# Optimization experiments

Hardware: AMD Instinct MI355X
Metric: run time of the kernel (lower is better)

## Reference

```python
import jax, jax.numpy as jnp
import numpy as np

INPUT_DIM, HIDDEN_DIM, OUTPUT_DIM = 64, 128, 1
BATCH, SEQ_LEN = 256, 512


def setup_inputs() -> dict:
    key = jax.random.key(0)
    ks = jax.random.split(key, 10)
    stdv = 1.0 / np.sqrt(HIDDEN_DIM)
    u = lambda k, shape: jax.random.uniform(k, shape, jnp.float32, -stdv, stdv)
    return {
        "X": jax.random.normal(ks[0], (BATCH, SEQ_LEN, INPUT_DIM), jnp.float32),
        "W": u(ks[1], (INPUT_DIM, 4 * HIDDEN_DIM)),
        "U": u(ks[2], (HIDDEN_DIM, 4 * HIDDEN_DIM)),
        "bias": u(ks[3], (4 * HIDDEN_DIM,)),
        "Wa": u(ks[4], (INPUT_DIM, INPUT_DIM)),
        "Ua": u(ks[5], (2 * HIDDEN_DIM, INPUT_DIM)),
        "ba": u(ks[6], (INPUT_DIM,)),
        "Va": u(ks[7], (INPUT_DIM, INPUT_DIM)),
        "fc_w": u(ks[8], (HIDDEN_DIM, OUTPUT_DIM)),
        "fc_b": u(ks[9], (OUTPUT_DIM,)),
    }


def reference(X, W, U, bias, Wa, Ua, ba, Va, fc_w, fc_b):
    B, T, _ = X.shape
    HS = U.shape[0]

    def step(carry, x_t):
        h, c = carry
        # variable attention over input features
        a_t = jnp.tanh(x_t @ Wa + jnp.concatenate([h, c], axis=1) @ Ua + ba) @ Va
        alpha_t = jax.nn.softmax(a_t, axis=1)
        xg = alpha_t * x_t
        gates = xg @ W + h @ U + bias
        i_t = jax.nn.sigmoid(gates[:, :HS])
        f_t = jax.nn.sigmoid(gates[:, HS:2 * HS])
        g_t = jnp.tanh(gates[:, 2 * HS:3 * HS])
        o_t = jax.nn.sigmoid(gates[:, 3 * HS:])
        c = f_t * c + i_t * g_t
        h = o_t * jnp.tanh(c)
        return (h, c), (h, alpha_t)

    h0 = jnp.zeros((B, HS), X.dtype)
    c0 = jnp.zeros((B, HS), X.dtype)
    (h_t, c_t), (hs, alphas) = jax.lax.scan(step, (h0, c0), jnp.swapaxes(X, 0, 1))
    hidden_seq = jnp.swapaxes(hs, 0, 1)  # [B, T, HS]
    y_pred = h_t @ fc_w + fc_b
    return y_pred, hidden_seq, (h_t, c_t), alphas[-1]
```

## Files before the change

kernel.cpp:

```cpp
#include <hip/hip_runtime.h>


#define TSEQ 512
#define NB   256
#define DIN  64
#define DHS  128
#define LOG2E 1.44269504f

typedef short bf16x8 __attribute__((ext_vector_type(8)));
typedef float f32x4  __attribute__((ext_vector_type(4)));

#define SWZ(off, row) ((off) ^ (((row) & 7) << 4))

__device__ __forceinline__ void bar_lds() {
  asm volatile("s_waitcnt lgkmcnt(0)\n\ts_barrier" ::: "memory");
}

__device__ __forceinline__ float fexp2(float x) { return __builtin_amdgcn_exp2f(x); }
__device__ __forceinline__ float frcp(float x)  { return __builtin_amdgcn_rcpf(x); }
__device__ __forceinline__ float sigm(float x)   { return frcp(1.0f + fexp2(-LOG2E * x)); }
__device__ __forceinline__ float tanh_f(float x) { return 1.0f - 2.0f * frcp(1.0f + fexp2(2.0f * LOG2E * x)); }

__device__ __forceinline__ unsigned short f2bf(float f) {
  return (unsigned short)((__float_as_uint(f) + 0x8000u) >> 16);
}
__device__ __forceinline__ unsigned int pack2(float a, float b) {
  return ((__float_as_uint(a) + 0x8000u) >> 16) | ((__float_as_uint(b) + 0x8000u) & 0xffff0000u);
}
__device__ __forceinline__ float bf2f(unsigned short u) {
  return __uint_as_float(((unsigned int)u) << 16);
}

__global__ __launch_bounds__(512, 2) void valstm_kernel(
    const float* __restrict__ X,  const float* __restrict__ W,  const float* __restrict__ U,
    const float* __restrict__ bias, const float* __restrict__ Wa, const float* __restrict__ Ua,
    const float* __restrict__ ba, const float* __restrict__ Va,
    const float* __restrict__ fcw, const float* __restrict__ fcb,
    float* __restrict__ out)
{
  const int tid = threadIdx.x;
  const int w   = tid >> 6;
  const int l   = tid & 63;
  const int lo  = l & 15;
  const int hi  = l >> 4;
  const int b0  = blockIdx.x * 16;

  __shared__ __align__(16) unsigned short hc[16 * 256];
  __shared__ __align__(16) unsigned short xbuf2[2][16 * 64];
  __shared__ __align__(16) unsigned short ta[16 * 64];
  __shared__ __align__(16) unsigned short ubuf[16 * 64];
  __shared__ __align__(16) float S4[64];
  __shared__ __align__(16) float hf[16 * 128];

  bf16x8 Uf[4][4];
  bf16x8 Wf[4][2];
  float  biasr[4];
  const int hid = 16 * w + lo;
  #pragma unroll
  for (int g = 0; g < 4; ++g) {
    const int j = g * 128 + hid;
    biasr[g] = bias[j];
    #pragma unroll
    for (int kt = 0; kt < 4; ++kt) {
      bf16x8 v;
      #pragma unroll
      for (int e = 0; e < 8; ++e) { const int k = kt * 32 + hi * 8 + e; v[e] = (short)f2bf(U[k * 512 + j]); }
      Uf[g][kt] = v;
    }
    #pragma unroll
    for (int kt = 0; kt < 2; ++kt) {
      bf16x8 v;
      #pragma unroll
      for (int e = 0; e < 8; ++e) { const int k = kt * 32 + hi * 8 + e; v[e] = (short)f2bf(W[k * 512 + j]); }
      Wf[g][kt] = v;
    }
  }

  bf16x8 Uaf[8], Waf[2], Vaf[2];
  float  bar = 0.0f;
  if (w < 4) {
    const int ja = 16 * w + lo;
    bar = ba[ja];
    #pragma unroll
    for (int kt = 0; kt < 8; ++kt) {
      bf16x8 v;
      #pragma unroll
      for (int e = 0; e < 8; ++e) { const int k = kt * 32 + hi * 8 + e; v[e] = (short)f2bf(Ua[k * 64 + ja]); }
      Uaf[kt] = v;
    }
    #pragma unroll
    for (int kt = 0; kt < 2; ++kt) {
      bf16x8 v;
      #pragma unroll
      for (int e = 0; e < 8; ++e) { const int k = kt * 32 + hi * 8 + e; v[e] = (short)f2bf(Wa[k * 64 + ja]); }
      Waf[kt] = v;
    }
    #pragma unroll
    for (int kt = 0; kt < 2; ++kt) {
      bf16x8 v;
      #pragma unroll
      for (int e = 0; e < 8; ++e) { const int k = kt * 32 + hi * 8 + e; v[e] = (short)f2bf(Va[k * 64 + ja]); }
      Vaf[kt] = v;
    }
  }

  int haf_off[4], caf_off[4], xa_off[2];
  #pragma unroll
  for (int kt = 0; kt < 4; ++kt) {
    haf_off[kt] = SWZ(lo * 512 + (kt * 32 + hi * 8) * 2, lo);
    caf_off[kt] = SWZ(lo * 512 + ((kt + 4) * 32 + hi * 8) * 2, lo);
  }
  #pragma unroll
  for (int kt = 0; kt < 2; ++kt)
    xa_off[kt] = SWZ(lo * 128 + (kt * 32 + hi * 8) * 2, lo);
  int ta_st[4], hc_h[4], hc_c[4];
  #pragma unroll
  for (int ri = 0; ri < 4; ++ri) {
    const int rr = hi * 4 + ri;
    ta_st[ri] = SWZ(rr * 128 + (16 * w + lo) * 2, rr);
    hc_h[ri]  = SWZ(rr * 512 + hid * 2, rr);
    hc_c[ri]  = SWZ(rr * 512 + (128 + hid) * 2, rr);
  }
  const int uq_off = SWZ(lo * 128 + (16 * w + hi * 4) * 2, lo);

  *(f32x4*)((char*)hc + tid * 16) = (f32x4){0.f, 0.f, 0.f, 0.f};

  const int xr = tid >> 5;
  const int xc = (tid & 31) * 2;
  const int xst_off = SWZ(xr * 128 + xc * 2, xr);
  const float* xptr = X + (size_t)(b0 + xr) * TSEQ * DIN + xc;
  {
    const float2 v0 = *(const float2*)(xptr + 0 * DIN);
    *(unsigned int*)((char*)xbuf2[0] + xst_off) = pack2(v0.x, v0.y);
  }
  float2 xf = *(const float2*)(xptr + 1 * DIN);

  float cst[4] = {0.f, 0.f, 0.f, 0.f};

  float* outY  = out;
  float* outHS = out + 256;
  float* outHT = out + 256 + (size_t)NB * TSEQ * DHS;
  float* outCT = outHT + NB * DHS;
  float* outAL = outCT + NB * DHS;

  float* hsP[4];
  #pragma unroll
  for (int ri = 0; ri < 4; ++ri)
    hsP[ri] = outHS + (size_t)(b0 + hi * 4 + ri) * TSEQ * DHS + hid;

  bar_lds();

  #pragma unroll 1
  for (int t = 0; t < TSEQ - 1; ++t) {
    const int xoff = (t & 1) << 11;

    bf16x8 haf[4];
    #pragma unroll
    for (int kt = 0; kt < 4; ++kt)
      haf[kt] = *(const bf16x8*)((const char*)hc + haf_off[kt]);

    f32x4 accU[4];
    unsigned long long xq = 0;

    if (w >= 4) {
      #pragma unroll
      for (int g = 0; g < 4; ++g) {
        accU[g] = (f32x4){biasr[g], biasr[g], biasr[g], biasr[g]};
        #pragma unroll
        for (int kt = 0; kt < 4; ++kt)
          accU[g] = __builtin_amdgcn_mfma_f32_16x16x32_bf16(haf[kt], Uf[g][kt], accU[g], 0, 0, 0);
      }
    }
    if (w < 4) {
      __builtin_amdgcn_s_setprio(1);
      xq = *(const unsigned long long*)((const char*)xbuf2[0] + xoff + uq_off);
      f32x4 aa = (f32x4){bar, bar, bar, bar};
      f32x4 ah = (f32x4){0.f, 0.f, 0.f, 0.f};
      f32x4 ac = (f32x4){0.f, 0.f, 0.f, 0.f};
      #pragma unroll
      for (int kt = 0; kt < 2; ++kt) {
        bf16x8 xa = *(const bf16x8*)((const char*)xbuf2[0] + xoff + xa_off[kt]);
        aa = __builtin_amdgcn_mfma_f32_16x16x32_bf16(xa, Waf[kt], aa, 0, 0, 0);
      }
      #pragma unroll
      for (int kt = 0; kt < 4; ++kt)
        ah = __builtin_amdgcn_mfma_f32_16x16x32_bf16(haf[kt], Uaf[kt], ah, 0, 0, 0);
      #pragma unroll
      for (int kt = 0; kt < 4; ++kt) {
        bf16x8 ca = *(const bf16x8*)((const char*)hc + caf_off[kt]);
        ac = __builtin_amdgcn_mfma_f32_16x16x32_bf16(ca, Uaf[kt + 4], ac, 0, 0, 0);
      }
      const f32x4 pre = aa + ah + ac;
      #pragma unroll
      for (int ri = 0; ri < 4; ++ri)
        *(unsigned short*)((char*)ta + ta_st[ri]) = f2bf(tanh_f(pre[ri]));
    }
    bar_lds();

    if (w < 4) {
      f32x4 av = (f32x4){0.f, 0.f, 0.f, 0.f};
      #pragma unroll
      for (int kt = 0; kt < 2; ++kt) {
        bf16x8 tf = *(const bf16x8*)((const char*)ta + xa_off[kt]);
        av = __builtin_amdgcn_mfma_f32_16x16x32_bf16(Vaf[kt], tf, av, 0, 0, 0);
      }
      f32x4 ev;
      #pragma unroll
      for (int ri = 0; ri < 4; ++ri) ev[ri] = fexp2(av[ri] * LOG2E);
      const unsigned int p0 = pack2(ev[0] * bf2f((unsigned short)xq),
                                    ev[1] * bf2f((unsigned short)(xq >> 16)));
      const unsigned int p1 = pack2(ev[2] * bf2f((unsigned short)(xq >> 32)),
                                    ev[3] * bf2f((unsigned short)(xq >> 48)));
      *(unsigned long long*)((char*)ubuf + uq_off) =
          (unsigned long long)p0 | ((unsigned long long)p1 << 32);
      float ps = ev[0] + ev[1] + ev[2] + ev[3];
      ps += __shfl_xor(ps, 16);
      ps += __shfl_xor(ps, 32);
      if (hi == 0) S4[lo * 4 + w] = ps;
      __builtin_amdgcn_s_setprio(0);
    }
    bar_lds();

    const bf16x8 uf0 = *(const bf16x8*)((const char*)ubuf + xa_off[0]);
    const bf16x8 uf1 = *(const bf16x8*)((const char*)ubuf + xa_off[1]);
    f32x4 s4r[4];
    #pragma unroll
    for (int ri = 0; ri < 4; ++ri)
      s4r[ri] = *(const f32x4*)(S4 + (hi * 4 + ri) * 4);

    if (w < 4) {
      #pragma unroll
      for (int g = 0; g < 4; ++g) {
        accU[g] = (f32x4){biasr[g], biasr[g], biasr[g], biasr[g]};
        #pragma unroll
        for (int kt = 0; kt < 4; ++kt)
          accU[g] = __builtin_amdgcn_mfma_f32_16x16x32_bf16(haf[kt], Uf[g][kt], accU[g], 0, 0, 0);
      }
    }
    f32x4 accW[4];
    #pragma unroll
    for (int g = 0; g < 4; ++g) accW[g] = (f32x4){0.f, 0.f, 0.f, 0.f};
    #pragma unroll
    for (int g = 0; g < 4; ++g)
      accW[g] = __builtin_amdgcn_mfma_f32_16x16x32_bf16(uf0, Wf[g][0], accW[g], 0, 0, 0);
    #pragma unroll
    for (int g = 0; g < 4; ++g)
      accW[g] = __builtin_amdgcn_mfma_f32_16x16x32_bf16(uf1, Wf[g][1], accW[g], 0, 0, 0);

    float rinv_[4];
    #pragma unroll
    for (int ri = 0; ri < 4; ++ri)
      rinv_[ri] = frcp(s4r[ri][0] + s4r[ri][1] + s4r[ri][2] + s4r[ri][3]);

    #pragma unroll
    for (int ri = 0; ri < 4; ++ri) {
      const float iv = sigm(accW[0][ri] * rinv_[ri] + accU[0][ri]);
      const float fv = sigm(accW[1][ri] * rinv_[ri] + accU[1][ri]);
      const float gv = tanh_f(accW[2][ri] * rinv_[ri] + accU[2][ri]);
      const float ov = sigm(accW[3][ri] * rinv_[ri] + accU[3][ri]);
      const float cn = fv * cst[ri] + iv * gv;
      const float hv = ov * tanh_f(cn);
      cst[ri] = cn;
      *(unsigned short*)((char*)hc + hc_h[ri]) = f2bf(hv);
      *(unsigned short*)((char*)hc + hc_c[ri]) = f2bf(cn);
      *hsP[ri] = hv;
      hsP[ri] += DHS;
    }

    {
      *(unsigned int*)((char*)xbuf2[0] + (((t + 1) & 1) << 11) + xst_off) = pack2(xf.x, xf.y);
      const int tn = (t + 2 < TSEQ) ? t + 2 : TSEQ - 1;
      xf = *(const float2*)(xptr + tn * DIN);
    }
    bar_lds();
  }

  {
    const int xoff = ((TSEQ - 1) & 1) << 11;

    bf16x8 haf[4];
    #pragma unroll
    for (int kt = 0; kt < 4; ++kt)
      haf[kt] = *(const bf16x8*)((const char*)hc + haf_off[kt]);

    if (w < 4) {
      f32x4 aa = (f32x4){bar, bar, bar, bar};
      f32x4 ah = (f32x4){0.f, 0.f, 0.f, 0.f};
      f32x4 ac = (f32x4){0.f, 0.f, 0.f, 0.f};
      #pragma unroll
      for (int kt = 0; kt < 2; ++kt) {
        bf16x8 xa = *(const bf16x8*)((const char*)xbuf2[0] + xoff + xa_off[kt]);
        aa = __builtin_amdgcn_mfma_f32_16x16x32_bf16(xa, Waf[kt], aa, 0, 0, 0);
      }
      #pragma unroll
      for (int kt = 0; kt < 4; ++kt)
        ah = __builtin_amdgcn_mfma_f32_16x16x32_bf16(haf[kt], Uaf[kt], ah, 0, 0, 0);
      #pragma unroll
      for (int kt = 0; kt < 4; ++kt) {
        bf16x8 ca = *(const bf16x8*)((const char*)hc + caf_off[kt]);
        ac = __builtin_amdgcn_mfma_f32_16x16x32_bf16(ca, Uaf[kt + 4], ac, 0, 0, 0);
      }
      const f32x4 pre = aa + ah + ac;
      #pragma unroll
      for (int ri = 0; ri < 4; ++ri)
        *(unsigned short*)((char*)ta + ta_st[ri]) = f2bf(tanh_f(pre[ri]));
    }
    bar_lds();

    f32x4 evP = (f32x4){0.f, 0.f, 0.f, 0.f};
    if (w < 4) {
      f32x4 av = (f32x4){0.f, 0.f, 0.f, 0.f};
      #pragma unroll
      for (int kt = 0; kt < 2; ++kt) {
        bf16x8 tf = *(const bf16x8*)((const char*)ta + xa_off[kt]);
        av = __builtin_amdgcn_mfma_f32_16x16x32_bf16(Vaf[kt], tf, av, 0, 0, 0);
      }
      #pragma unroll
      for (int ri = 0; ri < 4; ++ri) evP[ri] = fexp2(av[ri] * LOG2E);
      float ps = evP[0] + evP[1] + evP[2] + evP[3];
      ps += __shfl_xor(ps, 16);
      ps += __shfl_xor(ps, 32);
      const unsigned long long xq = *(const unsigned long long*)((const char*)xbuf2[0] + xoff + uq_off);
      const unsigned int p0 = pack2(evP[0] * bf2f((unsigned short)xq),
                                    evP[1] * bf2f((unsigned short)(xq >> 16)));
      const unsigned int p1 = pack2(evP[2] * bf2f((unsigned short)(xq >> 32)),
                                    evP[3] * bf2f((unsigned short)(xq >> 48)));
      *(unsigned long long*)((char*)ubuf + uq_off) =
          (unsigned long long)p0 | ((unsigned long long)p1 << 32);
      if (hi == 0) S4[lo * 4 + w] = ps;
    }
    f32x4 accU[4];
    #pragma unroll
    for (int g = 0; g < 4; ++g) {
      accU[g] = (f32x4){biasr[g], biasr[g], biasr[g], biasr[g]};
      #pragma unroll
      for (int kt = 0; kt < 4; ++kt)
        accU[g] = __builtin_amdgcn_mfma_f32_16x16x32_bf16(haf[kt], Uf[g][kt], accU[g], 0, 0, 0);
    }
    bar_lds();

    if (w < 4) {
      const f32x4 s4v = *(const f32x4*)(S4 + lo * 4);
      const float rA = frcp(s4v[0] + s4v[1] + s4v[2] + s4v[3]);
      *(f32x4*)(outAL + (b0 + lo) * 64 + 16 * w + hi * 4) =
          (f32x4){evP[0] * rA, evP[1] * rA, evP[2] * rA, evP[3] * rA};
    }

    f32x4 accW[4];
    #pragma unroll
    for (int g = 0; g < 4; ++g) accW[g] = (f32x4){0.f, 0.f, 0.f, 0.f};
    #pragma unroll
    for (int kt = 0; kt < 2; ++kt) {
      const bf16x8 uf = *(const bf16x8*)((const char*)ubuf + xa_off[kt]);
      #pragma unroll
      for (int g = 0; g < 4; ++g)
        accW[g] = __builtin_amdgcn_mfma_f32_16x16x32_bf16(uf, Wf[g][kt], accW[g], 0, 0, 0);
    }
    float rinv_[4];
    #pragma unroll
    for (int ri = 0; ri < 4; ++ri) {
      const f32x4 s4v = *(const f32x4*)(S4 + (hi * 4 + ri) * 4);
      rinv_[ri] = frcp(s4v[0] + s4v[1] + s4v[2] + s4v[3]);
    }
    #pragma unroll
    for (int ri = 0; ri < 4; ++ri) {
      const int rr = hi * 4 + ri;
      const float iv = sigm(accW[0][ri] * rinv_[ri] + accU[0][ri]);
      const float fv = sigm(accW[1][ri] * rinv_[ri] + accU[1][ri]);
      const float gv = tanh_f(accW[2][ri] * rinv_[ri] + accU[2][ri]);
      const float ov = sigm(accW[3][ri] * rinv_[ri] + accU[3][ri]);
      const float cn = fv * cst[ri] + iv * gv;
      const float hv = ov * tanh_f(cn);
      *(unsigned short*)((char*)hc + hc_h[ri]) = f2bf(hv);
      *(unsigned short*)((char*)hc + hc_c[ri]) = f2bf(cn);
      *hsP[ri] = hv;
      outHT[(b0 + rr) * DHS + hid] = hv;
      outCT[(b0 + rr) * DHS + hid] = cn;
      hf[rr * 128 + hid] = hv;
    }
  }
  bar_lds();

  if (w < 4) {
    const float fw0 = fcw[l], fw1 = fcw[64 + l];
    const float fb = fcb[0];
    #pragma unroll
    for (int rr = 0; rr < 4; ++rr) {
      const int r = w * 4 + rr;
      float s = hf[r * 128 + l] * fw0 + hf[r * 128 + 64 + l] * fw1;
      #pragma unroll
      for (int msk = 1; msk < 64; msk <<= 1) s += __shfl_xor(s, msk);
      if (l == 0) outY[b0 + r] = s + fb;
    }
  }
}

extern "C" void kernel_launch(void* const* d_in, const int* in_sizes, int n_in,
                              void* d_out, int out_size, void* d_ws, size_t ws_size,
                              hipStream_t stream) {
  const float* X    = (const float*)d_in[0];
  const float* W    = (const float*)d_in[1];
  const float* U    = (const float*)d_in[2];
  const float* bias = (const float*)d_in[3];
  const float* Wa   = (const float*)d_in[4];
  const float* Ua   = (const float*)d_in[5];
  const float* ba   = (const float*)d_in[6];
  const float* Va   = (const float*)d_in[7];
  const float* fcw  = (const float*)d_in[8];
  const float* fcb  = (const float*)d_in[9];
  valstm_kernel<<<16, 512, 0, stream>>>(X, W, U, bias, Wa, Ua, ba, Va, fcw, fcb, (float*)d_out);
}
```

Baseline: 996.9 us.

## Fold exp scale constants into weights and rebalance per-wave work in LSTM step

Pre-scales the gate, attention and Va weights and biases by log2e factors at load time, which removes per-element multiplies before the exp2 calls in activations. Moves the U-matrix MFMA for all waves into the slot between the attention phase and the barrier, so attention waves no longer compute it after the barrier. Gives the X prefetch (now float4 per thread) to the gate-only waves during the attention phase, taking it off the tail of every step. The pre-scaling happens before bf16 rounding, which slightly changes numerics.

```diff
diff --git a/kernel.cpp b/kernel.cpp
--- a/kernel.cpp
+++ b/kernel.cpp
@@ -9,6 +9,7 @@
 
 typedef short bf16x8 __attribute__((ext_vector_type(8)));
 typedef float f32x4  __attribute__((ext_vector_type(4)));
+typedef unsigned long long u64;
 
 #define SWZ(off, row) ((off) ^ (((row) & 7) << 4))
 
@@ -18,8 +19,9 @@
 
 __device__ __forceinline__ float fexp2(float x) { return __builtin_amdgcn_exp2f(x); }
 __device__ __forceinline__ float frcp(float x)  { return __builtin_amdgcn_rcpf(x); }
-__device__ __forceinline__ float sigm(float x)   { return frcp(1.0f + fexp2(-LOG2E * x)); }
-__device__ __forceinline__ float tanh_f(float x) { return 1.0f - 2.0f * frcp(1.0f + fexp2(2.0f * LOG2E * x)); }
+__device__ __forceinline__ float sig3(float x)  { return frcp(1.0f + fexp2(-x)); }
+__device__ __forceinline__ float tanh4(float x) { return 1.0f - 2.0f * frcp(1.0f + fexp2(x)); }
+__device__ __forceinline__ float tanh5(float y) { return 1.0f - 2.0f * frcp(1.0f + fexp2(2.0f * LOG2E * y)); }
 
 __device__ __forceinline__ unsigned short f2bf(float f) {
   return (unsigned short)((__float_as_uint(f) + 0x8000u) >> 16);
@@ -52,6 +54,7 @@
   __shared__ __align__(16) float S4[64];
   __shared__ __align__(16) float hf[16 * 128];
 
+  const float sgate[4] = {LOG2E, LOG2E, 2.0f * LOG2E, LOG2E};
   bf16x8 Uf[4][4];
   bf16x8 Wf[4][2];
   float  biasr[4];
@@ -59,19 +62,20 @@
   #pragma unroll
   for (int g = 0; g < 4; ++g) {
     const int j = g * 128 + hid;
-    biasr[g] = bias[j];
+    const float s = sgate[g];
+    biasr[g] = bias[j] * s;
     #pragma unroll
     for (int kt = 0; kt < 4; ++kt) {
       bf16x8 v;
       #pragma unroll
-      for (int e = 0; e < 8; ++e) { const int k = kt * 32 + hi * 8 + e; v[e] = (short)f2bf(U[k * 512 + j]); }
+      for (int e = 0; e < 8; ++e) { const int k = kt * 32 + hi * 8 + e; v[e] = (short)f2bf(U[k * 512 + j] * s); }
       Uf[g][kt] = v;
     }
     #pragma unroll
     for (int kt = 0; kt < 2; ++kt) {
       bf16x8 v;
       #pragma unroll
-      for (int e = 0; e < 8; ++e) { const int k = kt * 32 + hi * 8 + e; v[e] = (short)f2bf(W[k * 512 + j]); }
+      for (int e = 0; e < 8; ++e) { const int k = kt * 32 + hi * 8 + e; v[e] = (short)f2bf(W[k * 512 + j] * s); }
       Wf[g][kt] = v;
     }
   }
@@ -80,26 +84,27 @@
   float  bar = 0.0f;
   if (w < 4) {
     const int ja = 16 * w + lo;
-    bar = ba[ja];
+    const float SA = 2.0f * LOG2E;
+    bar = ba[ja] * SA;
     #pragma unroll
     for (int kt = 0; kt < 8; ++kt) {
       bf16x8 v;
       #pragma unroll
-      for (int e = 0; e < 8; ++e) { const int k = kt * 32 + hi * 8 + e; v[e] = (short)f2bf(Ua[k * 64 + ja]); }
+      for (int e = 0; e < 8; ++e) { const int k = kt * 32 + hi * 8 + e; v[e] = (short)f2bf(Ua[k * 64 + ja] * SA); }
       Uaf[kt] = v;
     }
     #pragma unroll
     for (int kt = 0; kt < 2; ++kt) {
       bf16x8 v;
       #pragma unroll
-      for (int e = 0; e < 8; ++e) { const int k = kt * 32 + hi * 8 + e; v[e] = (short)f2bf(Wa[k * 64 + ja]); }
+      for (int e = 0; e < 8; ++e) { const int k = kt * 32 + hi * 8 + e; v[e] = (short)f2bf(Wa[k * 64 + ja] * SA); }
       Waf[kt] = v;
     }
     #pragma unroll
     for (int kt = 0; kt < 2; ++kt) {
       bf16x8 v;
       #pragma unroll
-      for (int e = 0; e < 8; ++e) { const int k = kt * 32 + hi * 8 + e; v[e] = (short)f2bf(Va[k * 64 + ja]); }
+      for (int e = 0; e < 8; ++e) { const int k = kt * 32 + hi * 8 + e; v[e] = (short)f2bf(Va[k * 64 + ja] * LOG2E); }
       Vaf[kt] = v;
     }
   }
@@ -125,15 +130,18 @@
 
   *(f32x4*)((char*)hc + tid * 16) = (f32x4){0.f, 0.f, 0.f, 0.f};
 
-  const int xr = tid >> 5;
-  const int xc = (tid & 31) * 2;
-  const int xst_off = SWZ(xr * 128 + xc * 2, xr);
-  const float* xptr = X + (size_t)(b0 + xr) * TSEQ * DIN + xc;
-  {
-    const float2 v0 = *(const float2*)(xptr + 0 * DIN);
-    *(unsigned int*)((char*)xbuf2[0] + xst_off) = pack2(v0.x, v0.y);
-  }
-  float2 xf = *(const float2*)(xptr + 1 * DIN);
+  const int ct   = tid & 255;
+  const int xr4  = ct >> 4;
+  const int xc4  = (ct & 15) * 4;
+  const int xst4 = SWZ(xr4 * 128 + xc4 * 2, xr4);
+  const float* xp4 = X + (size_t)(b0 + xr4) * TSEQ * DIN + xc4;
+  float4 xf = {0.f, 0.f, 0.f, 0.f};
+  if (w >= 4) {
+    const float4 v0 = *(const float4*)(xp4);
+    *(u64*)((char*)xbuf2[0] + xst4) =
+        (u64)pack2(v0.x, v0.y) | ((u64)pack2(v0.z, v0.w) << 32);
+    xf = *(const float4*)(xp4 + DIN);
+  }
 
   float cst[4] = {0.f, 0.f, 0.f, 0.f};
 
@@ -159,21 +167,17 @@
     for (int kt = 0; kt < 4; ++kt)
       haf[kt] = *(const bf16x8*)((const char*)hc + haf_off[kt]);
 
-    f32x4 accU[4];
-    unsigned long long xq = 0;
+    u64 xq = 0;
 
     if (w >= 4) {
-      #pragma unroll
-      for (int g = 0; g < 4; ++g) {
-        accU[g] = (f32x4){biasr[g], biasr[g], biasr[g], biasr[g]};
-        #pragma unroll
-        for (int kt = 0; kt < 4; ++kt)
-          accU[g] = __builtin_amdgcn_mfma_f32_16x16x32_bf16(haf[kt], Uf[g][kt], accU[g], 0, 0, 0);
-      }
+      *(u64*)((char*)xbuf2[0] + (((t + 1) & 1) << 11) + xst4) =
+          (u64)pack2(xf.x, xf.y) | ((u64)pack2(xf.z, xf.w) << 32);
+      const int tn = (t + 2 < TSEQ) ? t + 2 : TSEQ - 1;
+      xf = *(const float4*)(xp4 + tn * DIN);
     }
     if (w < 4) {
       __builtin_amdgcn_s_setprio(1);
-      xq = *(const unsigned long long*)((const char*)xbuf2[0] + xoff + uq_off);
+      xq = *(const u64*)((const char*)xbuf2[0] + xoff + uq_off);
       f32x4 aa = (f32x4){bar, bar, bar, bar};
       f32x4 ah = (f32x4){0.f, 0.f, 0.f, 0.f};
       f32x4 ac = (f32x4){0.f, 0.f, 0.f, 0.f};
@@ -193,7 +197,7 @@
       const f32x4 pre = aa + ah + ac;
       #pragma unroll
       for (int ri = 0; ri < 4; ++ri)
-        *(unsigned short*)((char*)ta + ta_st[ri]) = f2bf(tanh_f(pre[ri]));
+        *(unsigned short*)((char*)ta + ta_st[ri]) = f2bf(tanh4(pre[ri]));
     }
     bar_lds();
 
@@ -206,19 +210,26 @@
       }
       f32x4 ev;
       #pragma unroll
-      for (int ri = 0; ri < 4; ++ri) ev[ri] = fexp2(av[ri] * LOG2E);
+      for (int ri = 0; ri < 4; ++ri) ev[ri] = fexp2(av[ri]);
       const unsigned int p0 = pack2(ev[0] * bf2f((unsigned short)xq),
                                     ev[1] * bf2f((unsigned short)(xq >> 16)));
       const unsigned int p1 = pack2(ev[2] * bf2f((unsigned short)(xq >> 32)),
                                     ev[3] * bf2f((unsigned short)(xq >> 48)));
-      *(unsigned long long*)((char*)ubuf + uq_off) =
-          (unsigned long long)p0 | ((unsigned long long)p1 << 32);
+      *(u64*)((char*)ubuf + uq_off) = (u64)p0 | ((u64)p1 << 32);
       float ps = ev[0] + ev[1] + ev[2] + ev[3];
       ps += __shfl_xor(ps, 16);
       ps += __shfl_xor(ps, 32);
       if (hi == 0) S4[lo * 4 + w] = ps;
       __builtin_amdgcn_s_setprio(0);
     }
+    f32x4 accU[4];
+    #pragma unroll
+    for (int g = 0; g < 4; ++g) {
+      accU[g] = (f32x4){biasr[g], biasr[g], biasr[g], biasr[g]};
+      #pragma unroll
+      for (int kt = 0; kt < 4; ++kt)
+        accU[g] = __builtin_amdgcn_mfma_f32_16x16x32_bf16(haf[kt], Uf[g][kt], accU[g], 0, 0, 0);
+    }
     bar_lds();
 
     const bf16x8 uf0 = *(const bf16x8*)((const char*)ubuf + xa_off[0]);
@@ -228,21 +239,11 @@
     for (int ri = 0; ri < 4; ++ri)
       s4r[ri] = *(const f32x4*)(S4 + (hi * 4 + ri) * 4);
 
-    if (w < 4) {
-      #pragma unroll
-      for (int g = 0; g < 4; ++g) {
-        accU[g] = (f32x4){biasr[g], biasr[g], biasr[g], biasr[g]};
-        #pragma unroll
-        for (int kt = 0; kt < 4; ++kt)
-          accU[g] = __builtin_amdgcn_mfma_f32_16x16x32_bf16(haf[kt], Uf[g][kt], accU[g], 0, 0, 0);
-      }
-    }
     f32x4 accW[4];
     #pragma unroll
-    for (int g = 0; g < 4; ++g) accW[g] = (f32x4){0.f, 0.f, 0.f, 0.f};
-    #pragma unroll
     for (int g = 0; g < 4; ++g)
-      accW[g] = __builtin_amdgcn_mfma_f32_16x16x32_bf16(uf0, Wf[g][0], accW[g], 0, 0, 0);
+      accW[g] = __builtin_amdgcn_mfma_f32_16x16x32_bf16(
+          uf0, Wf[g][0], (f32x4){0.f, 0.f, 0.f, 0.f}, 0, 0, 0);
     #pragma unroll
     for (int g = 0; g < 4; ++g)
       accW[g] = __builtin_amdgcn_mfma_f32_16x16x32_bf16(uf1, Wf[g][1], accW[g], 0, 0, 0);
@@ -254,24 +255,18 @@
 
     #pragma unroll
     for (int ri = 0; ri < 4; ++ri) {
-      const float iv = sigm(accW[0][ri] * rinv_[ri] + accU[0][ri]);
-      const float fv = sigm(accW[1][ri] * rinv_[ri] + accU[1][ri]);
-      const float gv = tanh_f(accW[2][ri] * rinv_[ri] + accU[2][ri]);
-      const float ov = sigm(accW[3][ri] * rinv_[ri] + accU[3][ri]);
+      const float iv = sig3(accW[0][ri] * rinv_[ri] + accU[0][ri]);
+      const float fv = sig3(accW[1][ri] * rinv_[ri] + accU[1][ri]);
+      const float gv = tanh4(accW[2][ri] * rinv_[ri] + accU[2][ri]);
+      const float ov = sig3(accW[3][ri] * rinv_[ri] + accU[3][ri]);
       const float cn = fv * cst[ri] + iv * gv;
-      const float hv = ov * tanh_f(cn);
+      const float hv = ov * tanh5(cn);
       cst[ri] = cn;
       *(unsigned short*)((char*)hc + hc_h[ri]) = f2bf(hv);
       *(unsigned short*)((char*)hc + hc_c[ri]) = f2bf(cn);
       *hsP[ri] = hv;
       hsP[ri] += DHS;
     }
-
-    {
-      *(unsigned int*)((char*)xbuf2[0] + (((t + 1) & 1) << 11) + xst_off) = pack2(xf.x, xf.y);
-      const int tn = (t + 2 < TSEQ) ? t + 2 : TSEQ - 1;
-      xf = *(const float2*)(xptr + tn * DIN);
-    }
     bar_lds();
   }
 
@@ -283,7 +278,9 @@
     for (int kt = 0; kt < 4; ++kt)
       haf[kt] = *(const bf16x8*)((const char*)hc + haf_off[kt]);
 
+    u64 xq = 0;
     if (w < 4) {
+      xq = *(const u64*)((const char*)xbuf2[0] + xoff + uq_off);
       f32x4 aa = (f32x4){bar, bar, bar, bar};
       f32x4 ah = (f32x4){0.f, 0.f, 0.f, 0.f};
       f32x4 ac = (f32x4){0.f, 0.f, 0.f, 0.f};
@@ -303,7 +300,7 @@
       const f32x4 pre = aa + ah + ac;
       #pragma unroll
       for (int ri = 0; ri < 4; ++ri)
-        *(unsigned short*)((char*)ta + ta_st[ri]) = f2bf(tanh_f(pre[ri]));
+        *(unsigned short*)((char*)ta + ta_st[ri]) = f2bf(tanh4(pre[ri]));
     }
     bar_lds();
 
@@ -316,17 +313,15 @@
         av = __builtin_amdgcn_mfma_f32_16x16x32_bf16(Vaf[kt], tf, av, 0, 0, 0);
       }
       #pragma unroll
-      for (int ri = 0; ri < 4; ++ri) evP[ri] = fexp2(av[ri] * LOG2E);
-      float ps = evP[0] + evP[1] + evP[2] + evP[3];
-      ps += __shfl_xor(ps, 16);
-      ps += __shfl_xor(ps, 32);
-      const unsigned long long xq = *(const unsigned long long*)((const char*)xbuf2[0] + xoff + uq_off);
+      for (int ri = 0; ri < 4; ++ri) evP[ri] = fexp2(av[ri]);
       const unsigned int p0 = pack2(evP[0] * bf2f((unsigned short)xq),
                                     evP[1] * bf2f((unsigned short)(xq >> 16)));
       const unsigned int p1 = pack2(evP[2] * bf2f((unsigned short)(xq >> 32)),
                                     evP[3] * bf2f((unsigned short)(xq >> 48)));
-      *(unsigned long long*)((char*)ubuf + uq_off) =
-          (unsigned long long)p0 | ((unsigned long long)p1 << 32);
+      *(u64*)((char*)ubuf + uq_off) = (u64)p0 | ((u64)p1 << 32);
+      float ps = evP[0] + evP[1] + evP[2] + evP[3];
+      ps += __shfl_xor(ps, 16);
+      ps += __shfl_xor(ps, 32);
       if (hi == 0) S4[lo * 4 + w] = ps;
     }
     f32x4 accU[4];
@@ -346,16 +341,17 @@
           (f32x4){evP[0] * rA, evP[1] * rA, evP[2] * rA, evP[3] * rA};
     }
 
+    const bf16x8 uf0 = *(const bf16x8*)((const char*)ubuf + xa_off[0]);
+    const bf16x8 uf1 = *(const bf16x8*)((const char*)ubuf + xa_off[1]);
     f32x4 accW[4];
     #pragma unroll
-    for (int g = 0; g < 4; ++g) accW[g] = (f32x4){0.f, 0.f, 0.f, 0.f};
-    #pragma unroll
-    for (int kt = 0; kt < 2; ++kt) {
-      const bf16x8 uf = *(const bf16x8*)((const char*)ubuf + xa_off[kt]);
-      #pragma unroll
-      for (int g = 0; g < 4; ++g)
-        accW[g] = __builtin_amdgcn_mfma_f32_16x16x32_bf16(uf, Wf[g][kt], accW[g], 0, 0, 0);
-    }
+    for (int g = 0; g < 4; ++g)
+      accW[g] = __builtin_amdgcn_mfma_f32_16x16x32_bf16(
+          uf0, Wf[g][0], (f32x4){0.f, 0.f, 0.f, 0.f}, 0, 0, 0);
+    #pragma unroll
+    for (int g = 0; g < 4; ++g)
+      accW[g] = __builtin_amdgcn_mfma_f32_16x16x32_bf16(uf1, Wf[g][1], accW[g], 0, 0, 0);
+
     float rinv_[4];
     #pragma unroll
     for (int ri = 0; ri < 4; ++ri) {
@@ -365,12 +361,12 @@
     #pragma unroll
     for (int ri = 0; ri < 4; ++ri) {
       const int rr = hi * 4 + ri;
-      const float iv = sigm(accW[0][ri] * rinv_[ri] + accU[0][ri]);
-      const float fv = sigm(accW[1][ri] * rinv_[ri] + accU[1][ri]);
-      const float gv = tanh_f(accW[2][ri] * rinv_[ri] + accU[2][ri]);
-      const float ov = sigm(accW[3][ri] * rinv_[ri] + accU[3][ri]);
+      const float iv = sig3(accW[0][ri] * rinv_[ri] + accU[0][ri]);
+      const float fv = sig3(accW[1][ri] * rinv_[ri] + accU[1][ri]);
+      const float gv = tanh4(accW[2][ri] * rinv_[ri] + accU[2][ri]);
+      const float ov = sig3(accW[3][ri] * rinv_[ri] + accU[3][ri]);
       const float cn = fv * cst[ri] + iv * gv;
-      const float hv = ov * tanh_f(cn);
+      const float hv = ov * tanh5(cn);
       *(unsigned short*)((char*)hc + hc_h[ri]) = f2bf(hv);
       *(unsigned short*)((char*)hc + hc_c[ri]) = f2bf(cn);
       *hsP[ri] = hv;
```

Result: slower. 1.351 ms (+35.5%).
